# Performance work log

Measured on AMD Instinct MI355X. Metric: run time of the kernel, lower is better.

The kernel has to match this reference:

```python
import jax, jax.numpy as jnp
import numpy as np

# CRF-RNN constants (DenseCRFParams defaults from crfasrnn_pytorch)
NUM_ITER = 5
NUM_LABELS = 2
ALPHA = 160.0   # bilateral spatial std
BETA = 3.0      # bilateral color std
GAMMA = 3.0     # spatial std
SPATIAL_W = 3.0
BILATERAL_W = 5.0
H = W = 96
EPS = 1e-20


def setup_inputs() -> dict:
    key = jax.random.key(0)
    k1, k2 = jax.random.split(key)
    image = jax.random.uniform(k1, (1, 3, H, W), dtype=jnp.float32) * 255.0  # raw RGB scale
    logits = jax.random.normal(k2, (1, NUM_LABELS, H, W), dtype=jnp.float32)
    eye = jnp.eye(NUM_LABELS, dtype=jnp.float32)
    return {
        "image": image,
        "logits": logits,
        "spatial_ker_weights": SPATIAL_W * eye,
        "bilateral_ker_weights": BILATERAL_W * eye,
        "compatibility_matrix": jnp.rot90(eye),
    }


def _gauss_kernel(f):
    # f: [N, D] features; K[i,j] = exp(-0.5 ||f_i - f_j||^2)
    sq = jnp.sum(f * f, axis=1)
    d = sq[:, None] + sq[None, :] - 2.0 * (f @ f.T)
    return jnp.exp(-0.5 * jnp.maximum(d, 0.0))


def _crf_single(image, logits, Wsp, Wbi, C):
    L, h, w = logits.shape
    N = h * w
    ys, xs = jnp.meshgrid(jnp.arange(h), jnp.arange(w), indexing="ij")
    pos = jnp.stack([ys, xs], axis=-1).reshape(N, 2).astype(logits.dtype)  # [N,2]
    rgb = image.reshape(3, N).T  # [N,3]

    Ksp = _gauss_kernel(pos / GAMMA)                                    # [N,N]
    Kbi = _gauss_kernel(jnp.concatenate([pos / ALPHA, rgb / BETA], 1))  # [N,N]
    # normalization: filter of all-ones image (permutohedral norm)
    nsp = 1.0 / (Ksp.sum(axis=1) + EPS)  # [N]
    nbi = 1.0 / (Kbi.sum(axis=1) + EPS)

    unary = logits.reshape(L, N)
    cur = unary
    for _ in range(NUM_ITER):
        q = jax.nn.softmax(cur, axis=0)          # [L,N]
        sp = (q @ Ksp) * nsp                     # normalized spatial filtering
        bi = (q @ Kbi) * nbi                     # normalized bilateral filtering
        msg = Wsp @ sp + Wbi @ bi                # [L,N]
        cur = unary - C @ msg                    # compatibility transform + update
    return cur.reshape(L, h, w)


def reference(image, logits, spatial_ker_weights, bilateral_ker_weights, compatibility_matrix):
    # image: [B,3,h,w], logits: [B,L,h,w] -> [B,L,h,w]
    return jax.vmap(_crf_single, in_axes=(0, 0, None, None, None))(
        image, logits, spatial_ker_weights, bilateral_ker_weights, compatibility_matrix
    )
```

## Files before the change

kernel.cpp:

```cpp
#include <hip/hip_runtime.h>
#include <hip/hip_fp16.h>
#include <math.h>

#define Hh 96
#define Ww 96
#define NPIX 9216
#define RAD 15
#define TAPS 31
#define NCH 144
#define NBIN 4096
#define GRIDB 2048
#define EPSV 1e-20f
#define LOG2E 1.4426950408889634f
#define CUT2 60.0f

#define OFF_F    0
#define OFF_Q0   73728
#define OFF_Q1   82944
#define OFF_QS   92160
#define OFF_CBI  101376
#define OFF_BV   110592
#define OFF_ROWW 119808
#define OFF_WTAB 119904
#define OFF_BBOX 119936
#define OFF_HIST 121664
#define OFF_BASE 125760
#define OFF_INV  129856
#define OFF_SRT  139072
#define OFF_OFS  148288
#define OFF_WORK 148433
#define OFF_K    169984

__device__ __forceinline__ int color_key(float r, float g, float b){
  int rq = min(15, (int)r >> 4);
  int gq = min(15, (int)g >> 4);
  int bq = min(15, (int)b >> 4);
  int key = 0;
  #pragma unroll
  for (int k=0;k<4;k++){
    key |= ((rq>>k)&1) << (3*k+2);
    key |= ((gq>>k)&1) << (3*k+1);
    key |= ((bq>>k)&1) << (3*k);
  }
  return key;
}

__global__ __launch_bounds__(256) void prepA_kernel(float* __restrict__ ws){
  int idx = blockIdx.x*256 + threadIdx.x;
  int* W = (int*)ws;
  if (idx < NPIX){ ws[OFF_BV+idx]=0.f; ws[OFF_CBI+idx]=0.f; }
  if (idx < NBIN) W[OFF_HIST+idx] = 0;
  if (blockIdx.x == 94 && threadIdx.x < Hh){
    int t = threadIdx.x;
    float s = 0.f;
    for (int yy=0; yy<Hh; ++yy){ float d=(float)(yy-t); s += expf(-d*d*(1.0f/18.0f)); }
    ws[OFF_ROWW + t] = s;
  }
  if (blockIdx.x == 95 && threadIdx.x < TAPS){
    int d = threadIdx.x - RAD;
    ws[OFF_WTAB + threadIdx.x] = expf(-(float)(d*d)*(1.0f/18.0f));
  }
}

__global__ __launch_bounds__(256) void prepB_kernel(const float* __restrict__ image,
                                                    float* __restrict__ ws){
  int n = blockIdx.x*256 + threadIdx.x;
  int key = color_key(image[n], image[NPIX+n], image[2*NPIX+n]);
  atomicAdd((int*)ws + OFF_HIST + key, 1);
}

__global__ __launch_bounds__(256) void prepC_kernel(float* __restrict__ ws){
  __shared__ int part[256];
  const int* hist = (const int*)ws + OFF_HIST;
  int* base = (int*)ws + OFF_BASE;
  int t = threadIdx.x;
  int loc[16]; int s = 0;
  #pragma unroll
  for (int i=0;i<16;i++){ loc[i]=s; s += hist[t*16+i]; }
  part[t] = s; __syncthreads();
  for (int off=1; off<256; off<<=1){
    int v = (t>=off) ? part[t-off] : 0;
    __syncthreads(); part[t] += v; __syncthreads();
  }
  int b = (t==0)?0:part[t-1];
  #pragma unroll
  for (int i=0;i<16;i++) base[t*16+i] = b + loc[i];
}

__global__ __launch_bounds__(256) void prepD_kernel(const float* __restrict__ image,
                                                    const float* __restrict__ logits,
                                                    float* __restrict__ ws){
  int n = blockIdx.x*256 + threadIdx.x;
  int* W = (int*)ws;
  float r=image[n], g=image[NPIX+n], bl=image[2*NPIX+n];
  int key = color_key(r,g,bl);
  int pos = atomicAdd(W + OFF_BASE + key, 1);
  W[OFF_INV + n] = pos;
  W[OFF_SRT + pos] = n;
  int y=n/Ww, x=n%Ww;
  const float c=0.7213475205f;
  const float sc=1.2011224088f;
  float f0=(float)y*(1.f/160.f), f1=(float)x*(1.f/160.f);
  float f2=r*(1.f/3.f), f3=g*(1.f/3.f), f4=bl*(1.f/3.f);
  float a=c*(f0*f0+f1*f1+f2*f2+f3*f3+f4*f4);
  float q = 1.f/(1.f + __builtin_amdgcn_exp2f((logits[NPIX+n]-logits[n])*LOG2E));
  float* F = ws + OFF_F + (size_t)pos*8;
  F[0]=sc*f0; F[1]=sc*f1; F[2]=sc*f2; F[3]=sc*f3; F[4]=sc*f4;
  F[5]=a; F[6]=0.f; F[7]=0.f;
  ws[OFF_Q0 + n] = q;
  ws[OFF_QS + pos] = q;
}

__global__ __launch_bounds__(256) void prepE1_kernel(float* __restrict__ ws){
  const int lane = threadIdx.x & 63, wid = threadIdx.x >> 6;
  int ch = blockIdx.x*4 + wid;
  if (ch >= NCH) return;
  const float* Fp = ws + OFF_F + ((size_t)ch*64 + lane)*8;
  float4 A = *(const float4*)Fp;
  float4 B4 = *(const float4*)(Fp+4);
  float mn[5]={A.x,A.y,A.z,A.w,B4.x}, mx[5]={A.x,A.y,A.z,A.w,B4.x};
  #pragma unroll
  for (int m=32; m; m>>=1){
    #pragma unroll
    for (int d=0;d<5;d++){
      mn[d]=fminf(mn[d], __shfl_xor(mn[d], m));
      mx[d]=fmaxf(mx[d], __shfl_xor(mx[d], m));
    }
  }
  if (lane == 0){
    float* bb = ws + OFF_BBOX + ch*12;
    #pragma unroll
    for (int d=0;d<5;d++){ bb[d]=mn[d]; bb[5+d]=mx[d]; }
  }
}

__global__ __launch_bounds__(256) void prepE2_kernel(float* __restrict__ ws){
  __shared__ float bbl[NCH*12];
  __shared__ int part[256];
  const int t = threadIdx.x, lane = t & 63, wid = t >> 6;
  int* W = (int*)ws;

  for (int i=t; i<NCH*12; i+=256) bbl[i] = ws[OFF_BBOX + i];
  __syncthreads();

  __shared__ int cnt[NCH];
  for (int jg = wid; jg < NCH; jg += 4){
    const float* jb = &bbl[jg*12];
    int base = 0;
    #pragma unroll
    for (int r2=0;r2<3;r2++){
      int c2 = lane + 64*r2;
      bool sv = false;
      if (c2 < NCH){
        const float* cb = &bbl[c2*12];
        float s2 = 0.f;
        #pragma unroll
        for (int d=0;d<5;d++){
          float gap = fmaxf(0.f, fmaxf(cb[d]-jb[5+d], jb[d]-cb[5+d]));
          s2 = fmaf(gap, gap, s2);
        }
        sv = (s2 <= CUT2);
      }
      base += __popcll(__ballot(sv));
    }
    if (lane == 0) cnt[jg] = base;
  }
  __syncthreads();

  int v = (t < NCH) ? cnt[t] : 0;
  part[t] = v; __syncthreads();
  for (int off=1; off<256; off<<=1){
    int u = (t>=off) ? part[t-off] : 0;
    __syncthreads(); part[t] += u; __syncthreads();
  }
  if (t == 0) W[OFF_OFS] = 0;
  if (t < NCH) W[OFF_OFS + t + 1] = part[t];
  __syncthreads();

  for (int jg = wid; jg < NCH; jg += 4){
    const float* jb = &bbl[jg*12];
    int base = (jg == 0) ? 0 : part[jg-1];
    #pragma unroll
    for (int r2=0;r2<3;r2++){
      int c2 = lane + 64*r2;
      bool sv = false;
      if (c2 < NCH){
        const float* cb = &bbl[c2*12];
        float s2 = 0.f;
        #pragma unroll
        for (int d=0;d<5;d++){
          float gap = fmaxf(0.f, fmaxf(cb[d]-jb[5+d], jb[d]-cb[5+d]));
          s2 = fmaf(gap, gap, s2);
        }
        sv = (s2 <= CUT2);
      }
      unsigned long long m = __ballot(sv);
      if (sv){
        int pos = __popcll(m & ((1ull<<lane)-1ull));
        W[OFF_WORK + base + pos] = (jg<<8) | c2;
      }
      base += __popcll(m);
    }
  }
}

__global__ __launch_bounds__(256) void buildK_kernel(float* __restrict__ ws){
  __shared__ float chunk[4][512];
  __shared__ float qsh[4][64];
  const int lane = threadIdx.x & 63, wid = threadIdx.x >> 6;
  int* W = (int*)ws;
  const int T = W[OFF_OFS + NCH];
  const int* work = W + OFF_WORK;
  const float* F  = ws + OFF_F;
  float* s = &chunk[wid][0];
  float* ql = &qsh[wid][0];
  for (int it = blockIdx.x*4 + wid; it < T; it += GRIDB*4){
    int en = work[it];
    int jg = en >> 8, c = en & 255;
    int js = jg*64 + lane;
    float4 A  = *(const float4*)(F + (size_t)js*8);
    float4 B4 = *(const float4*)(F + (size_t)js*8 + 4);
    float h0=A.x,h1=A.y,h2=A.z,h3=A.w,h4=B4.x,na=-B4.y;
    const float* src = F + (size_t)c*512;
    *(float4*)(s + lane*8)     = *(const float4*)(src + lane*8);
    *(float4*)(s + lane*8 + 4) = *(const float4*)(src + lane*8 + 4);
    ql[lane] = ws[OFF_QS + c*64 + lane];

    unsigned int kp[32];
    float aB=0.f, aC=0.f;
    #pragma unroll 4
    for (int ii=0; ii<32; ii++){
      float4 w0 = *(const float4*)(s + 2*ii*8);
      float4 w1 = *(const float4*)(s + 2*ii*8 + 4);
      float e0 = na - w1.y;
      e0=fmaf(h0,w0.x,e0); e0=fmaf(h1,w0.y,e0); e0=fmaf(h2,w0.z,e0);
      e0=fmaf(h3,w0.w,e0); e0=fmaf(h4,w1.x,e0);
      float k0 = __builtin_amdgcn_exp2f(e0);
      float4 u0 = *(const float4*)(s + (2*ii+1)*8);
      float4 u1 = *(const float4*)(s + (2*ii+1)*8 + 4);
      float e1 = na - u1.y;
      e1=fmaf(h0,u0.x,e1); e1=fmaf(h1,u0.y,e1); e1=fmaf(h2,u0.z,e1);
      e1=fmaf(h3,u0.w,e1); e1=fmaf(h4,u1.x,e1);
      float k1 = __builtin_amdgcn_exp2f(e1);
      aC += k0 + k1;
      aB = fmaf(k0, ql[2*ii],   aB);
      aB = fmaf(k1, ql[2*ii+1], aB);
      __half2 h2v = __floats2half2_rn(k0, k1);
      kp[ii] = *reinterpret_cast<unsigned int*>(&h2v);
    }
    unsigned int* Kp = (unsigned int*)ws + OFF_K + (size_t)it*2048 + lane*32;
    #pragma unroll
    for (int r=0;r<8;r++)
      *(uint4*)(Kp + r*4) = make_uint4(kp[4*r],kp[4*r+1],kp[4*r+2],kp[4*r+3]);
    atomicAdd(ws + OFF_BV  + js, aB);
    atomicAdd(ws + OFF_CBI + js, aC);
  }
}

__global__ __launch_bounds__(256) void matvec_kernel(float* __restrict__ ws){
  __shared__ float qsh[4][64];
  const int lane = threadIdx.x & 63, wid = threadIdx.x >> 6;
  const int* W = (const int*)ws;
  const int T = W[OFF_OFS + NCH];
  const int* work = W + OFF_WORK;
  float* ql = &qsh[wid][0];
  for (int it = blockIdx.x*4 + wid; it < T; it += GRIDB*4){
    int en = work[it];
    int jg = en >> 8, c = en & 255;
    int js = jg*64 + lane;
    ql[lane] = ws[OFF_QS + c*64 + lane];
    const unsigned int* Kp = (const unsigned int*)ws + OFF_K + (size_t)it*2048 + lane*32;
    float acc0=0.f, acc1=0.f;
    #pragma unroll
    for (int r=0;r<8;r++){
      uint4 p = *(const uint4*)(Kp + r*4);
      float4 qa = *(const float4*)(ql + r*8);
      float4 qb = *(const float4*)(ql + r*8 + 4);
      __half2 h;
      h = *reinterpret_cast<__half2*>(&p.x);
      acc0 = fmaf(__low2float(h), qa.x, acc0); acc1 = fmaf(__high2float(h), qa.y, acc1);
      h = *reinterpret_cast<__half2*>(&p.y);
      acc0 = fmaf(__low2float(h), qa.z, acc0); acc1 = fmaf(__high2float(h), qa.w, acc1);
      h = *reinterpret_cast<__half2*>(&p.z);
      acc0 = fmaf(__low2float(h), qb.x, acc0); acc1 = fmaf(__high2float(h), qb.y, acc1);
      h = *reinterpret_cast<__half2*>(&p.w);
      acc0 = fmaf(__low2float(h), qb.z, acc0); acc1 = fmaf(__high2float(h), qb.w, acc1);
    }
    atomicAdd(ws + OFF_BV + js, acc0 + acc1);
  }
}

__global__ __launch_bounds__(256) void combine_kernel(const float* __restrict__ logits,
                                                      const float* __restrict__ Wsp,
                                                      const float* __restrict__ Wbi,
                                                      const float* __restrict__ Cm,
                                                      float* __restrict__ ws,
                                                      float* __restrict__ out,
                                                      const float* __restrict__ qsrc,
                                                      float* __restrict__ qdst){
  __shared__ float tq[46][48];
  __shared__ float tr[46][17];
  __shared__ float wt[TAPS];
  int tx = threadIdx.x & 15, ty = threadIdx.x >> 4;
  int bx = blockIdx.x % 6, by = blockIdx.x / 6;
  int x0 = bx*16, y0 = by*16;

  for (int idx = threadIdx.x; idx < 46*46; idx += 256){
    int ly = idx / 46, lx = idx % 46;
    int gy = y0 - RAD + ly, gx = x0 - RAD + lx;
    float v = 0.f;
    if (gy >= 0 && gy < Hh && gx >= 0 && gx < Ww) v = qsrc[gy*Ww + gx];
    tq[ly][lx] = v;
  }
  if (threadIdx.x < TAPS) wt[threadIdx.x] = ws[OFF_WTAB + threadIdx.x];
  __syncthreads();

  for (int idx = threadIdx.x; idx < 46*16; idx += 256){
    int ly = idx >> 4, lx = idx & 15;
    float in = 0.f;
    #pragma unroll
    for (int dx=0; dx<TAPS; dx++) in = fmaf(wt[dx], tq[ly][lx+dx], in);
    tr[ly][lx] = in;
  }
  __syncthreads();

  int y = y0 + ty, x = x0 + tx, j = y*Ww + x;
  float S = 0.f;
  #pragma unroll
  for (int dy=0; dy<TAPS; dy++) S = fmaf(wt[dy], tr[ty+dy][tx], S);

  int js = ((const int*)ws)[OFF_INV + j];
  float Bv = ws[OFF_BV + js];
  ws[OFF_BV + js] = 0.f;
  float Cb = ws[OFF_CBI + js];
  float nb  = 1.0f/(Cb + EPSV);
  float Csp = ws[OFF_ROWW + y] * ws[OFF_ROWW + x];
  float nsp = 1.0f/(Csp + EPSV);

  float sp0 = S*nsp,  sp1 = (Csp - S)*nsp;
  float bi0 = Bv*nb,  bi1 = (Cb - Bv)*nb;

  float m0 = Wsp[0]*sp0 + Wsp[1]*sp1 + Wbi[0]*bi0 + Wbi[1]*bi1;
  float m1 = Wsp[2]*sp0 + Wsp[3]*sp1 + Wbi[2]*bi0 + Wbi[3]*bi1;
  float cm0 = Cm[0]*m0 + Cm[1]*m1;
  float cm1 = Cm[2]*m0 + Cm[3]*m1;

  float o0 = logits[j]        - cm0;
  float o1 = logits[NPIX + j] - cm1;
  out[j]        = o0;
  out[NPIX + j] = o1;

  float qn = 1.0f / (1.0f + __builtin_amdgcn_exp2f((o1-o0)*LOG2E));
  qdst[j] = qn;
  ws[OFF_QS + js] = qn;
}

extern "C" void kernel_launch(void* const* d_in, const int* in_sizes, int n_in,
                              void* d_out, int out_size, void* d_ws, size_t ws_size,
                              hipStream_t stream){
  const float* image  = (const float*)d_in[0];
  const float* logits = (const float*)d_in[1];
  const float* Wsp    = (const float*)d_in[2];
  const float* Wbi    = (const float*)d_in[3];
  const float* Cm     = (const float*)d_in[4];
  float* out = (float*)d_out;
  float* ws  = (float*)d_ws;

  float* qbuf[2] = { ws + OFF_Q0, ws + OFF_Q1 };

  prepA_kernel <<<96, 256, 0, stream>>>(ws);
  prepB_kernel <<<36, 256, 0, stream>>>(image, ws);
  prepC_kernel <<<1, 256, 0, stream>>>(ws);
  prepD_kernel <<<36, 256, 0, stream>>>(image, logits, ws);
  prepE1_kernel<<<36, 256, 0, stream>>>(ws);
  prepE2_kernel<<<1, 256, 0, stream>>>(ws);

  buildK_kernel<<<GRIDB, 256, 0, stream>>>(ws);
  combine_kernel<<<36, 256, 0, stream>>>(logits, Wsp, Wbi, Cm, ws, out,
                                         qbuf[0], qbuf[1]);
  for (int t=1; t<5; ++t){
    matvec_kernel<<<GRIDB, 256, 0, stream>>>(ws);
    combine_kernel<<<36, 256, 0, stream>>>(logits, Wsp, Wbi, Cm, ws, out,
                                           qbuf[t&1], qbuf[(t+1)&1]);
  }
}
```

Measured before the change: 145.9 us.

## Assign work per destination chunk and tighten bilateral cutoff radius

```diff
diff --git a/kernel.cpp b/kernel.cpp
--- a/kernel.cpp
+++ b/kernel.cpp
@@ -9,10 +9,10 @@
 #define TAPS 31
 #define NCH 144
 #define NBIN 4096
-#define GRIDB 2048
+#define SPLIT 4
 #define EPSV 1e-20f
 #define LOG2E 1.4426950408889634f
-#define CUT2 60.0f
+#define CUT2 42.0f
 
 #define OFF_F    0
 #define OFF_Q0   73728
@@ -137,13 +137,13 @@
 __global__ __launch_bounds__(256) void prepE2_kernel(float* __restrict__ ws){
   __shared__ float bbl[NCH*12];
   __shared__ int part[256];
+  __shared__ int cnt[NCH];
   const int t = threadIdx.x, lane = t & 63, wid = t >> 6;
   int* W = (int*)ws;
 
   for (int i=t; i<NCH*12; i+=256) bbl[i] = ws[OFF_BBOX + i];
   __syncthreads();
 
-  __shared__ int cnt[NCH];
   for (int jg = wid; jg < NCH; jg += 4){
     const float* jb = &bbl[jg*12];
     int base = 0;
@@ -197,7 +197,7 @@
       unsigned long long m = __ballot(sv);
       if (sv){
         int pos = __popcll(m & ((1ull<<lane)-1ull));
-        W[OFF_WORK + base + pos] = (jg<<8) | c2;
+        W[OFF_WORK + base + pos] = c2;
       }
       base += __popcll(m);
     }
@@ -208,40 +208,42 @@
   __shared__ float chunk[4][512];
   __shared__ float qsh[4][64];
   const int lane = threadIdx.x & 63, wid = threadIdx.x >> 6;
+  const int jg = blockIdx.x / SPLIT, sub = blockIdx.x % SPLIT;
   int* W = (int*)ws;
-  const int T = W[OFF_OFS + NCH];
+  const int b0 = W[OFF_OFS + jg], e0 = W[OFF_OFS + jg + 1];
   const int* work = W + OFF_WORK;
   const float* F  = ws + OFF_F;
   float* s = &chunk[wid][0];
   float* ql = &qsh[wid][0];
-  for (int it = blockIdx.x*4 + wid; it < T; it += GRIDB*4){
-    int en = work[it];
-    int jg = en >> 8, c = en & 255;
-    int js = jg*64 + lane;
-    float4 A  = *(const float4*)(F + (size_t)js*8);
-    float4 B4 = *(const float4*)(F + (size_t)js*8 + 4);
-    float h0=A.x,h1=A.y,h2=A.z,h3=A.w,h4=B4.x,na=-B4.y;
+
+  const int js = jg*64 + lane;
+  float4 A  = *(const float4*)(F + (size_t)js*8);
+  float4 B4 = *(const float4*)(F + (size_t)js*8 + 4);
+  const float h0=A.x,h1=A.y,h2=A.z,h3=A.w,h4=B4.x,na=-B4.y;
+
+  float aB=0.f, aC=0.f;
+  for (int it = b0 + sub*4 + wid; it < e0; it += 16){
+    int c = work[it];
     const float* src = F + (size_t)c*512;
     *(float4*)(s + lane*8)     = *(const float4*)(src + lane*8);
     *(float4*)(s + lane*8 + 4) = *(const float4*)(src + lane*8 + 4);
     ql[lane] = ws[OFF_QS + c*64 + lane];
 
     unsigned int kp[32];
-    float aB=0.f, aC=0.f;
     #pragma unroll 4
     for (int ii=0; ii<32; ii++){
       float4 w0 = *(const float4*)(s + 2*ii*8);
       float4 w1 = *(const float4*)(s + 2*ii*8 + 4);
-      float e0 = na - w1.y;
-      e0=fmaf(h0,w0.x,e0); e0=fmaf(h1,w0.y,e0); e0=fmaf(h2,w0.z,e0);
-      e0=fmaf(h3,w0.w,e0); e0=fmaf(h4,w1.x,e0);
-      float k0 = __builtin_amdgcn_exp2f(e0);
+      float e0v = na - w1.y;
+      e0v=fmaf(h0,w0.x,e0v); e0v=fmaf(h1,w0.y,e0v); e0v=fmaf(h2,w0.z,e0v);
+      e0v=fmaf(h3,w0.w,e0v); e0v=fmaf(h4,w1.x,e0v);
+      float k0 = __builtin_amdgcn_exp2f(e0v);
       float4 u0 = *(const float4*)(s + (2*ii+1)*8);
       float4 u1 = *(const float4*)(s + (2*ii+1)*8 + 4);
-      float e1 = na - u1.y;
-      e1=fmaf(h0,u0.x,e1); e1=fmaf(h1,u0.y,e1); e1=fmaf(h2,u0.z,e1);
-      e1=fmaf(h3,u0.w,e1); e1=fmaf(h4,u1.x,e1);
-      float k1 = __builtin_amdgcn_exp2f(e1);
+      float e1v = na - u1.y;
+      e1v=fmaf(h0,u0.x,e1v); e1v=fmaf(h1,u0.y,e1v); e1v=fmaf(h2,u0.z,e1v);
+      e1v=fmaf(h3,u0.w,e1v); e1v=fmaf(h4,u1.x,e1v);
+      float k1 = __builtin_amdgcn_exp2f(e1v);
       aC += k0 + k1;
       aB = fmaf(k0, ql[2*ii],   aB);
       aB = fmaf(k1, ql[2*ii+1], aB);
@@ -252,25 +254,26 @@
     #pragma unroll
     for (int r=0;r<8;r++)
       *(uint4*)(Kp + r*4) = make_uint4(kp[4*r],kp[4*r+1],kp[4*r+2],kp[4*r+3]);
-    atomicAdd(ws + OFF_BV  + js, aB);
-    atomicAdd(ws + OFF_CBI + js, aC);
-  }
+  }
+  atomicAdd(ws + OFF_BV  + js, aB);
+  atomicAdd(ws + OFF_CBI + js, aC);
 }
 
 __global__ __launch_bounds__(256) void matvec_kernel(float* __restrict__ ws){
   __shared__ float qsh[4][64];
   const int lane = threadIdx.x & 63, wid = threadIdx.x >> 6;
+  const int jg = blockIdx.x / SPLIT, sub = blockIdx.x % SPLIT;
   const int* W = (const int*)ws;
-  const int T = W[OFF_OFS + NCH];
+  const int b0 = W[OFF_OFS + jg], e0 = W[OFF_OFS + jg + 1];
   const int* work = W + OFF_WORK;
   float* ql = &qsh[wid][0];
-  for (int it = blockIdx.x*4 + wid; it < T; it += GRIDB*4){
-    int en = work[it];
-    int jg = en >> 8, c = en & 255;
-    int js = jg*64 + lane;
+  const int js = jg*64 + lane;
+
+  float acc0=0.f, acc1=0.f;
+  for (int it = b0 + sub*4 + wid; it < e0; it += 16){
+    int c = work[it];
     ql[lane] = ws[OFF_QS + c*64 + lane];
     const unsigned int* Kp = (const unsigned int*)ws + OFF_K + (size_t)it*2048 + lane*32;
-    float acc0=0.f, acc1=0.f;
     #pragma unroll
     for (int r=0;r<8;r++){
       uint4 p = *(const uint4*)(Kp + r*4);
@@ -286,8 +289,8 @@
       h = *reinterpret_cast<__half2*>(&p.w);
       acc0 = fmaf(__low2float(h), qb.z, acc0); acc1 = fmaf(__high2float(h), qb.w, acc1);
     }
-    atomicAdd(ws + OFF_BV + js, acc0 + acc1);
-  }
+  }
+  atomicAdd(ws + OFF_BV + js, acc0 + acc1);
 }
 
 __global__ __launch_bounds__(256) void combine_kernel(const float* __restrict__ logits,
@@ -375,11 +378,11 @@
   prepE1_kernel<<<36, 256, 0, stream>>>(ws);
   prepE2_kernel<<<1, 256, 0, stream>>>(ws);
 
-  buildK_kernel<<<GRIDB, 256, 0, stream>>>(ws);
+  buildK_kernel<<<NCH*SPLIT, 256, 0, stream>>>(ws);
   combine_kernel<<<36, 256, 0, stream>>>(logits, Wsp, Wbi, Cm, ws, out,
                                          qbuf[0], qbuf[1]);
   for (int t=1; t<5; ++t){
-    matvec_kernel<<<GRIDB, 256, 0, stream>>>(ws);
+    matvec_kernel<<<NCH*SPLIT, 256, 0, stream>>>(ws);
     combine_kernel<<<36, 256, 0, stream>>>(logits, Wsp, Wbi, Cm, ws, out,
                                            qbuf[t&1], qbuf[(t+1)&1]);
   }
```

Result: slower. 174.9 us (+19.9%).

## Software-pipeline buildK and matvec with contiguous per-wave work segments

Applied to the files above, without the earlier changes.

```diff
diff --git a/kernel.cpp b/kernel.cpp
--- a/kernel.cpp
+++ b/kernel.cpp
@@ -9,10 +9,11 @@
 #define TAPS 31
 #define NCH 144
 #define NBIN 4096
-#define GRIDB 2048
+#define GRIDK 256
+#define GRIDM 256
 #define EPSV 1e-20f
 #define LOG2E 1.4426950408889634f
-#define CUT2 60.0f
+#define CUT2 42.0f
 
 #define OFF_F    0
 #define OFF_Q0   73728
@@ -106,7 +107,7 @@
   float q = 1.f/(1.f + __builtin_amdgcn_exp2f((logits[NPIX+n]-logits[n])*LOG2E));
   float* F = ws + OFF_F + (size_t)pos*8;
   F[0]=sc*f0; F[1]=sc*f1; F[2]=sc*f2; F[3]=sc*f3; F[4]=sc*f4;
-  F[5]=a; F[6]=0.f; F[7]=0.f;
+  F[5]=a; F[6]=q; F[7]=0.f;
   ws[OFF_Q0 + n] = q;
   ws[OFF_QS + pos] = q;
 }
@@ -137,13 +138,13 @@
 __global__ __launch_bounds__(256) void prepE2_kernel(float* __restrict__ ws){
   __shared__ float bbl[NCH*12];
   __shared__ int part[256];
+  __shared__ int cnt[NCH];
   const int t = threadIdx.x, lane = t & 63, wid = t >> 6;
   int* W = (int*)ws;
 
   for (int i=t; i<NCH*12; i+=256) bbl[i] = ws[OFF_BBOX + i];
   __syncthreads();
 
-  __shared__ int cnt[NCH];
   for (int jg = wid; jg < NCH; jg += 4){
     const float* jb = &bbl[jg*12];
     int base = 0;
@@ -206,29 +207,49 @@
 
 __global__ __launch_bounds__(256) void buildK_kernel(float* __restrict__ ws){
   __shared__ float chunk[4][512];
-  __shared__ float qsh[4][64];
   const int lane = threadIdx.x & 63, wid = threadIdx.x >> 6;
   int* W = (int*)ws;
   const int T = W[OFF_OFS + NCH];
   const int* work = W + OFF_WORK;
   const float* F  = ws + OFF_F;
   float* s = &chunk[wid][0];
-  float* ql = &qsh[wid][0];
-  for (int it = blockIdx.x*4 + wid; it < T; it += GRIDB*4){
-    int en = work[it];
-    int jg = en >> 8, c = en & 255;
-    int js = jg*64 + lane;
-    float4 A  = *(const float4*)(F + (size_t)js*8);
-    float4 B4 = *(const float4*)(F + (size_t)js*8 + 4);
-    float h0=A.x,h1=A.y,h2=A.z,h3=A.w,h4=B4.x,na=-B4.y;
-    const float* src = F + (size_t)c*512;
-    *(float4*)(s + lane*8)     = *(const float4*)(src + lane*8);
-    *(float4*)(s + lane*8 + 4) = *(const float4*)(src + lane*8 + 4);
-    ql[lane] = ws[OFF_QS + c*64 + lane];
-
+  const int NW = GRIDK*4;
+  const int wv = blockIdx.x*4 + wid;
+  const int seg = (T + NW - 1)/NW;
+  int it = wv*seg;
+  const int itEnd = min(T, it + seg);
+  if (it >= itEnd) return;
+
+  int en = work[it];
+  int c = en & 255;
+  float4 rA = *(const float4*)(F + (size_t)c*512 + lane*8);
+  float4 rB = *(const float4*)(F + (size_t)c*512 + lane*8 + 4);
+  int js = (en >> 8)*64 + lane;
+  float4 jA = *(const float4*)(F + (size_t)js*8);
+  float4 jB = *(const float4*)(F + (size_t)js*8 + 4);
+
+  for (;;){
+    *(float4*)(s + lane*8)     = rA;
+    *(float4*)(s + lane*8 + 4) = rB;
+    const float h0=jA.x,h1=jA.y,h2=jA.z,h3=jA.w,h4=jB.x,na=-jB.y;
+    const int curIt = it, curJs = js;
+
+    int nit = it + 1;
+    bool more = nit < itEnd;
+    float4 nA, nB, njA, njB; int njs = 0;
+    if (more){
+      int en2 = work[nit];
+      int c2 = en2 & 255;
+      nA = *(const float4*)(F + (size_t)c2*512 + lane*8);
+      nB = *(const float4*)(F + (size_t)c2*512 + lane*8 + 4);
+      njs = (en2 >> 8)*64 + lane;
+      njA = *(const float4*)(F + (size_t)njs*8);
+      njB = *(const float4*)(F + (size_t)njs*8 + 4);
+    }
+
+    float aB=0.f, aC=0.f;
     unsigned int kp[32];
-    float aB=0.f, aC=0.f;
-    #pragma unroll 4
+    #pragma unroll
     for (int ii=0; ii<32; ii++){
       float4 w0 = *(const float4*)(s + 2*ii*8);
       float4 w1 = *(const float4*)(s + 2*ii*8 + 4);
@@ -243,17 +264,20 @@
       e1=fmaf(h3,u0.w,e1); e1=fmaf(h4,u1.x,e1);
       float k1 = __builtin_amdgcn_exp2f(e1);
       aC += k0 + k1;
-      aB = fmaf(k0, ql[2*ii],   aB);
-      aB = fmaf(k1, ql[2*ii+1], aB);
+      aB = fmaf(k0, w1.z, aB);
+      aB = fmaf(k1, u1.z, aB);
       __half2 h2v = __floats2half2_rn(k0, k1);
       kp[ii] = *reinterpret_cast<unsigned int*>(&h2v);
     }
-    unsigned int* Kp = (unsigned int*)ws + OFF_K + (size_t)it*2048 + lane*32;
+    unsigned int* Kp = (unsigned int*)ws + OFF_K + (size_t)curIt*2048 + lane*32;
     #pragma unroll
     for (int r=0;r<8;r++)
       *(uint4*)(Kp + r*4) = make_uint4(kp[4*r],kp[4*r+1],kp[4*r+2],kp[4*r+3]);
-    atomicAdd(ws + OFF_BV  + js, aB);
-    atomicAdd(ws + OFF_CBI + js, aC);
+    atomicAdd(ws + OFF_BV  + curJs, aB);
+    atomicAdd(ws + OFF_CBI + curJs, aC);
+
+    if (!more) break;
+    it = nit; js = njs; rA = nA; rB = nB; jA = njA; jB = njB;
   }
 }
 
@@ -264,29 +288,77 @@
   const int T = W[OFF_OFS + NCH];
   const int* work = W + OFF_WORK;
   float* ql = &qsh[wid][0];
-  for (int it = blockIdx.x*4 + wid; it < T; it += GRIDB*4){
-    int en = work[it];
-    int jg = en >> 8, c = en & 255;
-    int js = jg*64 + lane;
-    ql[lane] = ws[OFF_QS + c*64 + lane];
-    const unsigned int* Kp = (const unsigned int*)ws + OFF_K + (size_t)it*2048 + lane*32;
+  const int NW = GRIDM*4;
+  const int wv = blockIdx.x*4 + wid;
+  const int seg = (T + NW - 1)/NW;
+  int it = wv*seg;
+  const int itEnd = min(T, it + seg);
+  if (it >= itEnd) return;
+
+  const unsigned int* Kbase = (const unsigned int*)ws + OFF_K;
+
+  int en = work[it];
+  int c = en & 255;
+  int js = (en >> 8)*64 + lane;
+  float qv = ws[OFF_QS + c*64 + lane];
+  const unsigned int* Kp = Kbase + (size_t)it*2048 + lane*32;
+  uint4 p0 = *(const uint4*)(Kp);
+  uint4 p1 = *(const uint4*)(Kp + 4);
+  uint4 p2 = *(const uint4*)(Kp + 8);
+  uint4 p3 = *(const uint4*)(Kp + 12);
+  uint4 p4 = *(const uint4*)(Kp + 16);
+  uint4 p5 = *(const uint4*)(Kp + 20);
+  uint4 p6 = *(const uint4*)(Kp + 24);
+  uint4 p7 = *(const uint4*)(Kp + 28);
+
+  for (;;){
+    ql[lane] = qv;
+    const int curJs = js;
+
+    int nit = it + 1;
+    bool more = nit < itEnd;
+    float nqv = 0.f; int njs = 0;
+    uint4 n0,n1,n2,n3,n4,n5,n6,n7;
+    if (more){
+      int en2 = work[nit];
+      int c2 = en2 & 255;
+      njs = (en2 >> 8)*64 + lane;
+      nqv = ws[OFF_QS + c2*64 + lane];
+      const unsigned int* Np = Kbase + (size_t)nit*2048 + lane*32;
+      n0=*(const uint4*)(Np);    n1=*(const uint4*)(Np+4);
+      n2=*(const uint4*)(Np+8);  n3=*(const uint4*)(Np+12);
+      n4=*(const uint4*)(Np+16); n5=*(const uint4*)(Np+20);
+      n6=*(const uint4*)(Np+24); n7=*(const uint4*)(Np+28);
+    }
+
     float acc0=0.f, acc1=0.f;
-    #pragma unroll
-    for (int r=0;r<8;r++){
-      uint4 p = *(const uint4*)(Kp + r*4);
-      float4 qa = *(const float4*)(ql + r*8);
-      float4 qb = *(const float4*)(ql + r*8 + 4);
-      __half2 h;
-      h = *reinterpret_cast<__half2*>(&p.x);
-      acc0 = fmaf(__low2float(h), qa.x, acc0); acc1 = fmaf(__high2float(h), qa.y, acc1);
-      h = *reinterpret_cast<__half2*>(&p.y);
-      acc0 = fmaf(__low2float(h), qa.z, acc0); acc1 = fmaf(__high2float(h), qa.w, acc1);
-      h = *reinterpret_cast<__half2*>(&p.z);
-      acc0 = fmaf(__low2float(h), qb.x, acc0); acc1 = fmaf(__high2float(h), qb.y, acc1);
-      h = *reinterpret_cast<__half2*>(&p.w);
-      acc0 = fmaf(__low2float(h), qb.z, acc0); acc1 = fmaf(__high2float(h), qb.w, acc1);
-    }
-    atomicAdd(ws + OFF_BV + js, acc0 + acc1);
+    #define MV_STEP(P, R)                                                      \
+    {                                                                          \
+      float4 qa = *(const float4*)(ql + (R)*8);                                \
+      float4 qb = *(const float4*)(ql + (R)*8 + 4);                            \
+      __half2 h;                                                               \
+      h = *reinterpret_cast<__half2*>(&P.x);                                   \
+      acc0 = fmaf(__low2float(h), qa.x, acc0);                                 \
+      acc1 = fmaf(__high2float(h), qa.y, acc1);                                \
+      h = *reinterpret_cast<__half2*>(&P.y);                                   \
+      acc0 = fmaf(__low2float(h), qa.z, acc0);                                 \
+      acc1 = fmaf(__high2float(h), qa.w, acc1);                                \
+      h = *reinterpret_cast<__half2*>(&P.z);                                   \
+      acc0 = fmaf(__low2float(h), qb.x, acc0);                                 \
+      acc1 = fmaf(__high2float(h), qb.y, acc1);                                \
+      h = *reinterpret_cast<__half2*>(&P.w);                                   \
+      acc0 = fmaf(__low2float(h), qb.z, acc0);                                 \
+      acc1 = fmaf(__high2float(h), qb.w, acc1);                                \
+    }
+    MV_STEP(p0,0) MV_STEP(p1,1) MV_STEP(p2,2) MV_STEP(p3,3)
+    MV_STEP(p4,4) MV_STEP(p5,5) MV_STEP(p6,6) MV_STEP(p7,7)
+    #undef MV_STEP
+
+    atomicAdd(ws + OFF_BV + curJs, acc0 + acc1);
+
+    if (!more) break;
+    it = nit; js = njs; qv = nqv;
+    p0=n0; p1=n1; p2=n2; p3=n3; p4=n4; p5=n5; p6=n6; p7=n7;
   }
 }
 
@@ -375,11 +447,11 @@
   prepE1_kernel<<<36, 256, 0, stream>>>(ws);
   prepE2_kernel<<<1, 256, 0, stream>>>(ws);
 
-  buildK_kernel<<<GRIDB, 256, 0, stream>>>(ws);
+  buildK_kernel<<<GRIDK, 256, 0, stream>>>(ws);
   combine_kernel<<<36, 256, 0, stream>>>(logits, Wsp, Wbi, Cm, ws, out,
                                          qbuf[0], qbuf[1]);
   for (int t=1; t<5; ++t){
-    matvec_kernel<<<GRIDB, 256, 0, stream>>>(ws);
+    matvec_kernel<<<GRIDM, 256, 0, stream>>>(ws);
     combine_kernel<<<36, 256, 0, stream>>>(logits, Wsp, Wbi, Cm, ws, out,
                                            qbuf[t&1], qbuf[(t+1)&1]);
   }
```

Measured after the change: 157.0 us, median of 2. +7.6%, slower.

## Tighten bilateral cutoff, coalesce fp16 kernel storage, pack q into features

Applied to the files above, without the earlier changes.

```diff
diff --git a/kernel.cpp b/kernel.cpp
--- a/kernel.cpp
+++ b/kernel.cpp
@@ -12,7 +12,7 @@
 #define GRIDB 2048
 #define EPSV 1e-20f
 #define LOG2E 1.4426950408889634f
-#define CUT2 60.0f
+#define CUT2 42.0f
 
 #define OFF_F    0
 #define OFF_Q0   73728
@@ -26,10 +26,9 @@
 #define OFF_HIST 121664
 #define OFF_BASE 125760
 #define OFF_INV  129856
-#define OFF_SRT  139072
-#define OFF_OFS  148288
-#define OFF_WORK 148433
-#define OFF_K    169984
+#define OFF_OFS  139072
+#define OFF_WORK 139217
+#define OFF_K    165888
 
 __device__ __forceinline__ int color_key(float r, float g, float b){
   int rq = min(15, (int)r >> 4);
@@ -96,7 +95,6 @@
   int key = color_key(r,g,bl);
   int pos = atomicAdd(W + OFF_BASE + key, 1);
   W[OFF_INV + n] = pos;
-  W[OFF_SRT + pos] = n;
   int y=n/Ww, x=n%Ww;
   const float c=0.7213475205f;
   const float sc=1.2011224088f;
@@ -106,7 +104,7 @@
   float q = 1.f/(1.f + __builtin_amdgcn_exp2f((logits[NPIX+n]-logits[n])*LOG2E));
   float* F = ws + OFF_F + (size_t)pos*8;
   F[0]=sc*f0; F[1]=sc*f1; F[2]=sc*f2; F[3]=sc*f3; F[4]=sc*f4;
-  F[5]=a; F[6]=0.f; F[7]=0.f;
+  F[5]=a; F[6]=q; F[7]=0.f;
   ws[OFF_Q0 + n] = q;
   ws[OFF_QS + pos] = q;
 }
@@ -137,13 +135,13 @@
 __global__ __launch_bounds__(256) void prepE2_kernel(float* __restrict__ ws){
   __shared__ float bbl[NCH*12];
   __shared__ int part[256];
+  __shared__ int cnt[NCH];
   const int t = threadIdx.x, lane = t & 63, wid = t >> 6;
   int* W = (int*)ws;
 
   for (int i=t; i<NCH*12; i+=256) bbl[i] = ws[OFF_BBOX + i];
   __syncthreads();
 
-  __shared__ int cnt[NCH];
   for (int jg = wid; jg < NCH; jg += 4){
     const float* jb = &bbl[jg*12];
     int base = 0;
@@ -206,28 +204,28 @@
 
 __global__ __launch_bounds__(256) void buildK_kernel(float* __restrict__ ws){
   __shared__ float chunk[4][512];
-  __shared__ float qsh[4][64];
   const int lane = threadIdx.x & 63, wid = threadIdx.x >> 6;
   int* W = (int*)ws;
   const int T = W[OFF_OFS + NCH];
   const int* work = W + OFF_WORK;
   const float* F  = ws + OFF_F;
+  unsigned int* Kb = (unsigned int*)ws + OFF_K;
   float* s = &chunk[wid][0];
-  float* ql = &qsh[wid][0];
+
   for (int it = blockIdx.x*4 + wid; it < T; it += GRIDB*4){
     int en = work[it];
     int jg = en >> 8, c = en & 255;
     int js = jg*64 + lane;
-    float4 A  = *(const float4*)(F + (size_t)js*8);
-    float4 B4 = *(const float4*)(F + (size_t)js*8 + 4);
-    float h0=A.x,h1=A.y,h2=A.z,h3=A.w,h4=B4.x,na=-B4.y;
+    float4 jA = *(const float4*)(F + (size_t)js*8);
+    float4 jB = *(const float4*)(F + (size_t)js*8 + 4);
+    const float h0=jA.x,h1=jA.y,h2=jA.z,h3=jA.w,h4=jB.x,na=-jB.y;
+
     const float* src = F + (size_t)c*512;
     *(float4*)(s + lane*8)     = *(const float4*)(src + lane*8);
     *(float4*)(s + lane*8 + 4) = *(const float4*)(src + lane*8 + 4);
-    ql[lane] = ws[OFF_QS + c*64 + lane];
-
-    unsigned int kp[32];
-    float aB=0.f, aC=0.f;
+
+    float aB0=0.f,aB1=0.f,aC0=0.f,aC1=0.f;
+    unsigned int* Kit = Kb + (size_t)it*2048 + lane;
     #pragma unroll 4
     for (int ii=0; ii<32; ii++){
       float4 w0 = *(const float4*)(s + 2*ii*8);
@@ -242,18 +240,14 @@
       e1=fmaf(h0,u0.x,e1); e1=fmaf(h1,u0.y,e1); e1=fmaf(h2,u0.z,e1);
       e1=fmaf(h3,u0.w,e1); e1=fmaf(h4,u1.x,e1);
       float k1 = __builtin_amdgcn_exp2f(e1);
-      aC += k0 + k1;
-      aB = fmaf(k0, ql[2*ii],   aB);
-      aB = fmaf(k1, ql[2*ii+1], aB);
-      __half2 h2v = __floats2half2_rn(k0, k1);
-      kp[ii] = *reinterpret_cast<unsigned int*>(&h2v);
-    }
-    unsigned int* Kp = (unsigned int*)ws + OFF_K + (size_t)it*2048 + lane*32;
-    #pragma unroll
-    for (int r=0;r<8;r++)
-      *(uint4*)(Kp + r*4) = make_uint4(kp[4*r],kp[4*r+1],kp[4*r+2],kp[4*r+3]);
-    atomicAdd(ws + OFF_BV  + js, aB);
-    atomicAdd(ws + OFF_CBI + js, aC);
+      aC0 += k0; aC1 += k1;
+      aB0 = fmaf(k0, w1.z, aB0);
+      aB1 = fmaf(k1, u1.z, aB1);
+      __half2 hv = __floats2half2_rn(k0, k1);
+      Kit[ii*64] = *reinterpret_cast<unsigned int*>(&hv);
+    }
+    atomicAdd(ws + OFF_BV  + js, aB0 + aB1);
+    atomicAdd(ws + OFF_CBI + js, aC0 + aC1);
   }
 }
 
@@ -263,30 +257,24 @@
   const int* W = (const int*)ws;
   const int T = W[OFF_OFS + NCH];
   const int* work = W + OFF_WORK;
+  const unsigned int* Kb = (const unsigned int*)ws + OFF_K;
   float* ql = &qsh[wid][0];
+
   for (int it = blockIdx.x*4 + wid; it < T; it += GRIDB*4){
     int en = work[it];
-    int jg = en >> 8, c = en & 255;
-    int js = jg*64 + lane;
+    int c = en & 255;
+    int js = (en >> 8)*64 + lane;
     ql[lane] = ws[OFF_QS + c*64 + lane];
-    const unsigned int* Kp = (const unsigned int*)ws + OFF_K + (size_t)it*2048 + lane*32;
-    float acc0=0.f, acc1=0.f;
-    #pragma unroll
-    for (int r=0;r<8;r++){
-      uint4 p = *(const uint4*)(Kp + r*4);
-      float4 qa = *(const float4*)(ql + r*8);
-      float4 qb = *(const float4*)(ql + r*8 + 4);
-      __half2 h;
-      h = *reinterpret_cast<__half2*>(&p.x);
-      acc0 = fmaf(__low2float(h), qa.x, acc0); acc1 = fmaf(__high2float(h), qa.y, acc1);
-      h = *reinterpret_cast<__half2*>(&p.y);
-      acc0 = fmaf(__low2float(h), qa.z, acc0); acc1 = fmaf(__high2float(h), qa.w, acc1);
-      h = *reinterpret_cast<__half2*>(&p.z);
-      acc0 = fmaf(__low2float(h), qb.x, acc0); acc1 = fmaf(__high2float(h), qb.y, acc1);
-      h = *reinterpret_cast<__half2*>(&p.w);
-      acc0 = fmaf(__low2float(h), qb.z, acc0); acc1 = fmaf(__high2float(h), qb.w, acc1);
-    }
-    atomicAdd(ws + OFF_BV + js, acc0 + acc1);
+    const unsigned int* Kit = Kb + (size_t)it*2048 + lane;
+    float a0=0.f, a1=0.f;
+    #pragma unroll 8
+    for (int ii=0; ii<32; ii++){
+      unsigned int kk = Kit[ii*64];
+      __half2 hv = *reinterpret_cast<__half2*>(&kk);
+      a0 = fmaf(__low2float(hv),  ql[2*ii],   a0);
+      a1 = fmaf(__high2float(hv), ql[2*ii+1], a1);
+    }
+    atomicAdd(ws + OFF_BV + js, a0 + a1);
   }
 }
 
```

Result: faster. 130.5 us (median of 2 runs) (-10.5%).
